# Optimization experiments

Hardware: AMD Instinct MI355X
Metric: run time of the kernel (lower is better)

## Reference

```python
import jax, jax.numpy as jnp
import numpy as np

N, D, V = 2048, 128, 131072
B, T = 8, 256
U_DECAY, X_DECAY, THR = 0.97, 0.97, 0.02


def _ln(z, eps=1e-6):
    # row-wise layernorm matching torch: std with ddof=1 (unbiased)
    m = z.mean(-1, keepdims=True)
    s = jnp.sqrt(((z - m) ** 2).sum(-1, keepdims=True) / (z.shape[-1] - 1))
    return (z - m) / (s + eps)


def setup_inputs() -> dict:
    key = jax.random.key(0)
    k = jax.random.split(key, 5)
    E = jax.random.normal(k[0], (D, N), dtype=jnp.float32) / N ** 0.5
    Dx = jax.random.normal(k[1], (N, D), dtype=jnp.float32) / D ** 0.5
    Dy = jax.random.normal(k[2], (N, D), dtype=jnp.float32) / D ** 0.5
    token_emb = jax.random.normal(k[3], (V, D), dtype=jnp.float32) / D ** 0.5
    tokens = jax.random.randint(k[4], (B, T), 0, V)
    return {"E": E, "Dx": Dx, "Dy": Dy, "token_emb": token_emb, "tokens": tokens}


def reference(E, Dx, Dy, token_emb, tokens):
    Bc, Tc = tokens.shape
    n, d = Dx.shape[0], Dx.shape[1]
    x0 = jnp.zeros((Bc, n), dtype=E.dtype)
    rho0 = jnp.zeros((Bc, d, n), dtype=E.dtype)

    def cell(carry, tok):
        x, rho = carry
        v_prev = token_emb[tok]                             # [B,d]
        xt = X_DECAY * x + v_prev @ Dx.T                    # [B,n]
        xt = xt / (jnp.abs(xt).sum(-1, keepdims=True) + 1e-6)
        thr = THR * xt.max(-1, keepdims=True)
        xt = jnp.where(xt > thr, xt, 0.0)                   # sparsifying threshold
        a_star = jnp.einsum('bdn,bn->bd', rho, xt)          # fast-weight read
        y_core = _ln(a_star) @ Dy.T                         # ln_before_Dy=True -> [B,n]
        yt = jnp.maximum(y_core, 0.0) * jnp.maximum(xt, 0.0)
        v_star = _ln(yt @ E.T)                              # [B,d]
        rho = U_DECAY * (rho + v_prev[:, :, None] * xt[:, None, :])  # rank-1 update + decay
        return (xt, rho), v_star

    (_, _), v_seq = jax.lax.scan(cell, (x0, rho0), tokens.T)  # v_seq: [T,B,d]
    return jnp.transpose(v_seq, (1, 0, 2))                    # [B,T,d]
```

## Files before the change

kernel.cpp:

```cpp
#include <hip/hip_runtime.h>

typedef unsigned int u32;
typedef unsigned short u16;

#define T_SEQ 256
#define N_DIM 2048
#define D_DIM 128
#define B_BATCH 8

typedef __attribute__((ext_vector_type(8))) short bfrag;
typedef __attribute__((ext_vector_type(4))) float f4acc;

__device__ __forceinline__ u16 f2bf(float f) {
  u32 u = __float_as_uint(f);
  return (u16)((u + 0x7FFFu + ((u >> 16) & 1u)) >> 16);
}
__device__ __forceinline__ float bf2f(u16 h) { return __uint_as_float(((u32)h) << 16); }

__global__ __launch_bounds__(128) void k_gather(const float* __restrict__ emb,
                                                const int* __restrict__ toks,
                                                float* __restrict__ Vp) {
  int r = blockIdx.x;
  int d = threadIdx.x;
  int tok = toks[r];
  Vp[(long)r * D_DIM + d] = emb[(long)tok * D_DIM + d];
}

__global__ __launch_bounds__(256) void k_cast(const float* __restrict__ src,
                                              u16* __restrict__ dst, int n) {
  for (int i = blockIdx.x * 256 + threadIdx.x; i < n; i += gridDim.x * 256)
    dst[i] = f2bf(src[i]);
}

__global__ __launch_bounds__(256) void k_zero(float* __restrict__ p, long n4) {
  long i = (long)blockIdx.x * blockDim.x + threadIdx.x;
  if (i < n4) ((float4*)p)[i] = make_float4(0.f, 0.f, 0.f, 0.f);
}

__global__ __launch_bounds__(256) void k_gemm_abT(
    const float* __restrict__ A, const float* __restrict__ Bm, float* __restrict__ C,
    int M, int N, int K) {
  constexpr int BM = 64, BN = 64, BK = 16;
  __shared__ float As[BK][BM + 4];
  __shared__ float Bs[BK][BN + 4];
  int tid = threadIdx.x;
  int tx = tid & 15, ty = tid >> 4;
  int row0 = blockIdx.y * BM, col0 = blockIdx.x * BN;
  float acc[4][4] = {};

  for (int k0 = 0; k0 < K; k0 += BK) {
#pragma unroll
    for (int i = 0; i < 4; i++) {
      int idx = tid + i * 256;
      int m = idx >> 4;
      int k = idx & 15;
      As[k][m] = A[(long)(row0 + m) * K + k0 + k];
      Bs[k][m] = Bm[(long)(col0 + m) * K + k0 + k];
    }
    __syncthreads();
#pragma unroll
    for (int k = 0; k < BK; k++) {
      float a[4], b[4];
#pragma unroll
      for (int i = 0; i < 4; i++) a[i] = As[k][ty * 4 + i];
#pragma unroll
      for (int j = 0; j < 4; j++) b[j] = Bs[k][tx * 4 + j];
#pragma unroll
      for (int i = 0; i < 4; i++)
#pragma unroll
        for (int j = 0; j < 4; j++) acc[i][j] += a[i] * b[j];
    }
    __syncthreads();
  }
#pragma unroll
  for (int i = 0; i < 4; i++) {
    long off = (long)(row0 + ty * 4 + i) * N + col0 + tx * 4;
    *(float4*)(C + off) = make_float4(acc[i][0], acc[i][1], acc[i][2], acc[i][3]);
  }
}

template <int EPI, int TRI>
__global__ __launch_bounds__(256) void k_mfma_abT(
    const u16* __restrict__ A, const u16* __restrict__ Bm, void* __restrict__ Cv,
    const u16* __restrict__ Xr, int M, int N, int K, int KS,
    long sA, long sB, long sC) {
  int bz = blockIdx.z;
  int batch = bz / KS, ks = bz - batch * KS;
  int row0 = blockIdx.y * 64, col0 = blockIdx.x * 64;
  if (TRI && col0 > row0) return;
  A += (long)batch * sA;
  Bm += (long)batch * sB;
  int kLen = K / KS, k0beg = ks * kLen;

  __shared__ __align__(16) u16 As[64 * 64];
  __shared__ __align__(16) u16 Bs[64 * 64];
  int tid = threadIdx.x;
  int w = tid >> 6, lane = tid & 63;
  int qr = (w >> 1) * 32, qc = (w & 1) * 32;
  int l15 = lane & 15, lhi = lane >> 4;

  f4acc acc[2][2];
#pragma unroll
  for (int i = 0; i < 2; i++)
#pragma unroll
    for (int j = 0; j < 2; j++)
#pragma unroll
      for (int e = 0; e < 4; e++) acc[i][j][e] = 0.f;

  for (int k0 = k0beg; k0 < k0beg + kLen; k0 += 64) {
    __syncthreads();
#pragma unroll
    for (int p = 0; p < 2; p++) {
      int idx = tid + p * 256;
      int r = idx >> 3, c8 = (idx & 7) * 8;
      uint4 av = *(const uint4*)(A + (long)(row0 + r) * K + k0 + c8);
      uint4 bv = *(const uint4*)(Bm + (long)(col0 + r) * K + k0 + c8);
      int sw = (c8 * 2) ^ ((r & 7) << 4);
      *(uint4*)((char*)As + r * 128 + sw) = av;
      *(uint4*)((char*)Bs + r * 128 + sw) = bv;
    }
    __syncthreads();
#pragma unroll
    for (int kk = 0; kk < 2; kk++) {
      bfrag af[2], bf[2];
      int cb = kk * 64 + lhi * 16;
#pragma unroll
      for (int f = 0; f < 2; f++) {
        int ra = qr + f * 16 + l15;
        af[f] = *(const bfrag*)((const char*)As + ra * 128 + (cb ^ ((ra & 7) << 4)));
        int rb = qc + f * 16 + l15;
        bf[f] = *(const bfrag*)((const char*)Bs + rb * 128 + (cb ^ ((rb & 7) << 4)));
      }
#pragma unroll
      for (int i = 0; i < 2; i++)
#pragma unroll
        for (int j = 0; j < 2; j++)
          acc[i][j] = __builtin_amdgcn_mfma_f32_16x16x32_bf16(af[i], bf[j], acc[i][j], 0, 0, 0);
    }
  }

#pragma unroll
  for (int i = 0; i < 2; i++)
#pragma unroll
    for (int j = 0; j < 2; j++) {
      int rbase = row0 + qr + i * 16 + lhi * 4;
      int c = col0 + qc + j * 16 + l15;
#pragma unroll
      for (int e = 0; e < 4; e++) {
        long r = rbase + e;
        float v = acc[i][j][e];
        if (EPI == 0) {
          unsafeAtomicAdd((float*)Cv + (long)batch * sC + r * N + c, v);
        } else {
          float xv = bf2f(Xr[r * (long)N + c]);
          ((u16*)Cv)[r * (long)N + c] = f2bf(fmaxf(v, 0.f) * fmaxf(xv, 0.f));
        }
      }
    }
}

template <int CTRL>
__device__ __forceinline__ float dpp_mov(float v) {
  return __int_as_float(
      __builtin_amdgcn_update_dpp(0, __float_as_int(v), CTRL, 0xF, 0xF, true));
}

__device__ __forceinline__ void wave_reduce_sum_max63(float& s, float& m) {
  s += dpp_mov<0x111>(s);  m = fmaxf(m, dpp_mov<0x111>(m));
  s += dpp_mov<0x112>(s);  m = fmaxf(m, dpp_mov<0x112>(m));
  s += dpp_mov<0x114>(s);  m = fmaxf(m, dpp_mov<0x114>(m));
  s += dpp_mov<0x118>(s);  m = fmaxf(m, dpp_mov<0x118>(m));
  s += dpp_mov<0x142>(s);  m = fmaxf(m, dpp_mov<0x142>(m));
  s += dpp_mov<0x143>(s);  m = fmaxf(m, dpp_mov<0x143>(m));
}

__device__ __forceinline__ float wave_sum63(float s) {
  s += dpp_mov<0x111>(s);
  s += dpp_mov<0x112>(s);
  s += dpp_mov<0x114>(s);
  s += dpp_mov<0x118>(s);
  s += dpp_mov<0x142>(s);
  s += dpp_mov<0x143>(s);
  return s;
}

__global__ __launch_bounds__(256) void k_scan(const float* __restrict__ P,
                                              u16* __restrict__ Xb) {
  int b = blockIdx.x;
  int tid = threadIdx.x;
  int wave = tid >> 6;
  int lane = tid & 63;
  __shared__ float red[2][4][2];

  const float4* Pv = (const float4*)(P + (long)b * T_SEQ * N_DIM);
  u16* Xrow = Xb + (long)b * T_SEQ * N_DIM;
  const int ROWQ = N_DIM / 4;
  const long o0 = (long)tid * 2, o1 = o0 + 1;

  float x[8];
#pragma unroll
  for (int j = 0; j < 8; j++) x[j] = 0.f;

  auto rowOff = [&](int t) { return (long)(t < T_SEQ ? t : T_SEQ - 1) * ROWQ; };

  auto step = [&](const float4& v0, const float4& v1, int t) {
    float z[8];
    z[0] = 0.97f * x[0] + v0.x;
    z[1] = 0.97f * x[1] + v0.y;
    z[2] = 0.97f * x[2] + v0.z;
    z[3] = 0.97f * x[3] + v0.w;
    z[4] = 0.97f * x[4] + v1.x;
    z[5] = 0.97f * x[5] + v1.y;
    z[6] = 0.97f * x[6] + v1.z;
    z[7] = 0.97f * x[7] + v1.w;
    float s0 = fabsf(z[0]) + fabsf(z[4]);
    float s1 = fabsf(z[1]) + fabsf(z[5]);
    float s2 = fabsf(z[2]) + fabsf(z[6]);
    float s3 = fabsf(z[3]) + fabsf(z[7]);
    float m0 = fmaxf(z[0], z[4]);
    float m1 = fmaxf(z[1], z[5]);
    float m2 = fmaxf(z[2], z[6]);
    float m3 = fmaxf(z[3], z[7]);
    float s = (s0 + s1) + (s2 + s3);
    float m = fmaxf(fmaxf(m0, m1), fmaxf(m2, m3));
    wave_reduce_sum_max63(s, m);
    int par = t & 1;
    if (lane == 63) {
      red[par][wave][0] = s;
      red[par][wave][1] = m;
    }
    __syncthreads();
    float S = (red[par][0][0] + red[par][1][0]) + (red[par][2][0] + red[par][3][0]);
    float M = fmaxf(fmaxf(red[par][0][1], red[par][1][1]),
                    fmaxf(red[par][2][1], red[par][3][1]));
    float inv = 1.f / (S + 1e-6f);
    float thr = 0.02f * M;
#pragma unroll
    for (int j = 0; j < 8; j++) x[j] = (z[j] > thr) ? z[j] * inv : 0.f;
    uint4 pk;
    pk.x = (u32)f2bf(x[0]) | ((u32)f2bf(x[1]) << 16);
    pk.y = (u32)f2bf(x[2]) | ((u32)f2bf(x[3]) << 16);
    pk.z = (u32)f2bf(x[4]) | ((u32)f2bf(x[5]) << 16);
    pk.w = (u32)f2bf(x[6]) | ((u32)f2bf(x[7]) << 16);
    *(uint4*)(Xrow + (long)t * N_DIM + tid * 8) = pk;
  };

  float4 A0 = Pv[rowOff(0) + o0], A1 = Pv[rowOff(0) + o1];
  float4 B0 = Pv[rowOff(1) + o0], B1 = Pv[rowOff(1) + o1];
  float4 C0 = Pv[rowOff(2) + o0], C1 = Pv[rowOff(2) + o1];
  float4 D0, D1;

  for (int t = 0; t < T_SEQ; t += 4) {
    D0 = Pv[rowOff(t + 3) + o0];
    D1 = Pv[rowOff(t + 3) + o1];
    step(A0, A1, t);
    A0 = Pv[rowOff(t + 4) + o0];
    A1 = Pv[rowOff(t + 4) + o1];
    step(B0, B1, t + 1);
    B0 = Pv[rowOff(t + 5) + o0];
    B1 = Pv[rowOff(t + 5) + o1];
    step(C0, C1, t + 2);
    C0 = Pv[rowOff(t + 6) + o0];
    C1 = Pv[rowOff(t + 6) + o1];
    step(D0, D1, t + 3);
  }
}

__global__ __launch_bounds__(128) void k_astar_ln(const float* __restrict__ S,
                                                  const float* __restrict__ Vp,
                                                  u16* __restrict__ LnAb) {
  int bx = blockIdx.x;
  int b = bx >> 8, t = bx & 255;
  int d = threadIdx.x;
  int wave = d >> 6, lane = d & 63;
  __shared__ float redS[2], redV[2];
  const float* Sb = S + ((long)b * T_SEQ + t) * T_SEQ;
  const float* Vb = Vp + (long)b * T_SEQ * D_DIM;
  float acc = 0.f;
  float w = 1.f;
  for (int s = t - 1; s >= 0; s--) {
    w *= 0.97f;
    acc += w * Sb[s] * Vb[(long)s * D_DIM + d];
  }
  float s1 = wave_sum63(acc);
  if (lane == 63) redS[wave] = s1;
  __syncthreads();
  float mean = (redS[0] + redS[1]) * (1.f / 128.f);
  float dv = acc - mean;
  float v = wave_sum63(dv * dv);
  if (lane == 63) redV[wave] = v;
  __syncthreads();
  float sd = sqrtf((redV[0] + redV[1]) * (1.f / 127.f));
  LnAb[((long)b * T_SEQ + t) * D_DIM + d] = f2bf(dv / (sd + 1e-6f));
}

__global__ __launch_bounds__(64) void k_ln(const float* __restrict__ In,
                                           float* __restrict__ Out) {
  long base = (long)blockIdx.x * D_DIM;
  int lane = threadIdx.x;
  float a = In[base + lane];
  float b = In[base + lane + 64];
  float s = a + b;
#pragma unroll
  for (int off = 32; off >= 1; off >>= 1) s += __shfl_xor(s, off);
  float m = s * (1.f / 128.f);
  float da = a - m, db = b - m;
  float v = da * da + db * db;
#pragma unroll
  for (int off = 32; off >= 1; off >>= 1) v += __shfl_xor(v, off);
  float sd = sqrtf(v * (1.f / 127.f));
  float invs = 1.f / (sd + 1e-6f);
  Out[base + lane] = da * invs;
  Out[base + lane + 64] = db * invs;
}

extern "C" void kernel_launch(void* const* d_in, const int* in_sizes, int n_in,
                              void* d_out, int out_size, void* d_ws, size_t ws_size,
                              hipStream_t stream) {
  const float* E = (const float*)d_in[0];
  const float* Dx = (const float*)d_in[1];
  const float* Dy = (const float*)d_in[2];
  const float* emb = (const float*)d_in[3];
  const int* toks = (const int*)d_in[4];
  float* out = (float*)d_out;

  char* ws = (char*)d_ws;
  const size_t MB = 1u << 20;
  float* Vp = (float*)(ws + 0 * MB);
  float* P = (float*)(ws + 1 * MB);
  u16* Ytb = (u16*)(ws + 1 * MB);
  u16* Xb = (u16*)(ws + 17 * MB);
  float* S = (float*)(ws + 25 * MB);
  float* U = (float*)(ws + 27 * MB);
  u16* LnAb = (u16*)(ws + 28 * MB);
  u16* Dyb = (u16*)(ws + 29 * MB);
  u16* Eb = (u16*)(ws + 30 * MB);

  const int R = B_BATCH * T_SEQ;

  k_gather<<<R, D_DIM, 0, stream>>>(emb, toks, Vp);
  k_cast<<<256, 256, 0, stream>>>(Dy, Dyb, N_DIM * D_DIM);
  k_cast<<<256, 256, 0, stream>>>(E, Eb, N_DIM * D_DIM);
  k_gemm_abT<<<dim3(N_DIM / 64, R / 64, 1), 256, 0, stream>>>(
      Vp, Dx, P, R, N_DIM, D_DIM);
  k_scan<<<B_BATCH, 256, 0, stream>>>(P, Xb);
  k_zero<<<768, 256, 0, stream>>>(S, 3L * MB / 16);
  k_mfma_abT<0, 1><<<dim3(4, 4, B_BATCH * 4), 256, 0, stream>>>(
      Xb, Xb, S, nullptr, T_SEQ, T_SEQ, N_DIM, 4,
      (long)T_SEQ * N_DIM, (long)T_SEQ * N_DIM, (long)T_SEQ * T_SEQ);
  k_astar_ln<<<R, D_DIM, 0, stream>>>(S, Vp, LnAb);
  k_mfma_abT<1, 0><<<dim3(N_DIM / 64, R / 64, 1), 256, 0, stream>>>(
      LnAb, Dyb, Ytb, Xb, R, N_DIM, D_DIM, 1, 0, 0, 0);
  k_mfma_abT<0, 0><<<dim3(D_DIM / 64, R / 64, 8), 256, 0, stream>>>(
      Ytb, Eb, U, nullptr, R, D_DIM, N_DIM, 8, 0, 0, 0);
  k_ln<<<R, 64, 0, stream>>>(U, out);
}
```

Baseline: 297.9 us.

## Use split-bf16 MFMA for P projection and LDS-staged async loads in scan

Replaces the fp32 SIMT GEMM computing V·Dx^T with a bf16 MFMA kernel that splits each operand into high and low bf16 parts and sums three products, keeping accuracy close to fp32. This adds a cast kernel for Dx and writes hi/lo copies in the gather kernel. The serial scan kernel now prefetches rows of P into a triple-buffered LDS ring via global_load_lds, with explicit waitcnt and barriers replacing the register prefetch. The goal is to cut GEMM compute time and hide load latency in the latency-bound scan, at the cost of extra casting passes and hand-managed synchronization.

```diff
diff --git a/kernel.cpp b/kernel.cpp
--- a/kernel.cpp
+++ b/kernel.cpp
@@ -17,13 +17,25 @@
 }
 __device__ __forceinline__ float bf2f(u16 h) { return __uint_as_float(((u32)h) << 16); }
 
+__device__ __forceinline__ void stage16(const void* g, void* l) {
+  __builtin_amdgcn_global_load_lds(
+      (const __attribute__((address_space(1))) void*)g,
+      (__attribute__((address_space(3))) void*)l, 16, 0, 0);
+}
+
 __global__ __launch_bounds__(128) void k_gather(const float* __restrict__ emb,
                                                 const int* __restrict__ toks,
-                                                float* __restrict__ Vp) {
+                                                float* __restrict__ Vp,
+                                                u16* __restrict__ Vph,
+                                                u16* __restrict__ Vpl) {
   int r = blockIdx.x;
   int d = threadIdx.x;
-  int tok = toks[r];
-  Vp[(long)r * D_DIM + d] = emb[(long)tok * D_DIM + d];
+  float v = emb[(long)toks[r] * D_DIM + d];
+  long o = (long)r * D_DIM + d;
+  Vp[o] = v;
+  u16 h = f2bf(v);
+  Vph[o] = h;
+  Vpl[o] = f2bf(v - bf2f(h));
 }
 
 __global__ __launch_bounds__(256) void k_cast(const float* __restrict__ src,
@@ -32,51 +44,91 @@
     dst[i] = f2bf(src[i]);
 }
 
+__global__ __launch_bounds__(256) void k_cast2(const float* __restrict__ src,
+                                               u16* __restrict__ h,
+                                               u16* __restrict__ l, int n) {
+  for (int i = blockIdx.x * 256 + threadIdx.x; i < n; i += gridDim.x * 256) {
+    float v = src[i];
+    u16 hh = f2bf(v);
+    h[i] = hh;
+    l[i] = f2bf(v - bf2f(hh));
+  }
+}
+
 __global__ __launch_bounds__(256) void k_zero(float* __restrict__ p, long n4) {
   long i = (long)blockIdx.x * blockDim.x + threadIdx.x;
   if (i < n4) ((float4*)p)[i] = make_float4(0.f, 0.f, 0.f, 0.f);
 }
 
-__global__ __launch_bounds__(256) void k_gemm_abT(
-    const float* __restrict__ A, const float* __restrict__ Bm, float* __restrict__ C,
-    int M, int N, int K) {
-  constexpr int BM = 64, BN = 64, BK = 16;
-  __shared__ float As[BK][BM + 4];
-  __shared__ float Bs[BK][BN + 4];
+__global__ __launch_bounds__(256) void k_mfma_p(
+    const u16* __restrict__ Ah, const u16* __restrict__ Al,
+    const u16* __restrict__ Bh, const u16* __restrict__ Bl,
+    float* __restrict__ C) {
+  __shared__ __align__(16) u16 sA[2][64 * 128];
+  __shared__ __align__(16) u16 sB[2][64 * 128];
   int tid = threadIdx.x;
-  int tx = tid & 15, ty = tid >> 4;
-  int row0 = blockIdx.y * BM, col0 = blockIdx.x * BN;
-  float acc[4][4] = {};
-
-  for (int k0 = 0; k0 < K; k0 += BK) {
-#pragma unroll
-    for (int i = 0; i < 4; i++) {
-      int idx = tid + i * 256;
-      int m = idx >> 4;
-      int k = idx & 15;
-      As[k][m] = A[(long)(row0 + m) * K + k0 + k];
-      Bs[k][m] = Bm[(long)(col0 + m) * K + k0 + k];
-    }
-    __syncthreads();
-#pragma unroll
-    for (int k = 0; k < BK; k++) {
-      float a[4], b[4];
-#pragma unroll
-      for (int i = 0; i < 4; i++) a[i] = As[k][ty * 4 + i];
-#pragma unroll
-      for (int j = 0; j < 4; j++) b[j] = Bs[k][tx * 4 + j];
-#pragma unroll
-      for (int i = 0; i < 4; i++)
-#pragma unroll
-        for (int j = 0; j < 4; j++) acc[i][j] += a[i] * b[j];
-    }
-    __syncthreads();
-  }
-#pragma unroll
-  for (int i = 0; i < 4; i++) {
-    long off = (long)(row0 + ty * 4 + i) * N + col0 + tx * 4;
-    *(float4*)(C + off) = make_float4(acc[i][0], acc[i][1], acc[i][2], acc[i][3]);
-  }
+  int w = tid >> 6, lane = tid & 63;
+  int qr = (w >> 1) * 32, qc = (w & 1) * 32;
+  int l15 = lane & 15, lhi = lane >> 4;
+  int row0 = blockIdx.y * 64, col0 = blockIdx.x * 64;
+
+  f4acc acc[2][2];
+#pragma unroll
+  for (int i = 0; i < 2; i++)
+#pragma unroll
+    for (int j = 0; j < 2; j++)
+#pragma unroll
+      for (int e = 0; e < 4; e++) acc[i][j][e] = 0.f;
+
+#pragma unroll
+  for (int hl = 0; hl < 2; hl++) {
+    const u16* A = hl ? Al : Ah;
+    const u16* B = hl ? Bl : Bh;
+#pragma unroll
+    for (int p = 0; p < 4; p++) {
+      int idx = tid + p * 256;
+      int r = idx >> 4, ch = idx & 15;
+      int off = r * 256 + ((ch * 16) ^ ((r & 7) << 4));
+      *(uint4*)((char*)sA[hl] + off) = *(const uint4*)(A + (long)(row0 + r) * D_DIM + ch * 8);
+      *(uint4*)((char*)sB[hl] + off) = *(const uint4*)(B + (long)(col0 + r) * D_DIM + ch * 8);
+    }
+  }
+  __syncthreads();
+
+#pragma unroll
+  for (int kk = 0; kk < 4; kk++) {
+    bfrag ah[2], al[2], bh[2], bl[2];
+    int cb = kk * 64 + lhi * 16;
+#pragma unroll
+    for (int f = 0; f < 2; f++) {
+      int ra = qr + f * 16 + l15, rb = qc + f * 16 + l15;
+      int oa = ra * 256 + (cb ^ ((ra & 7) << 4));
+      int ob = rb * 256 + (cb ^ ((rb & 7) << 4));
+      ah[f] = *(const bfrag*)((const char*)sA[0] + oa);
+      al[f] = *(const bfrag*)((const char*)sA[1] + oa);
+      bh[f] = *(const bfrag*)((const char*)sB[0] + ob);
+      bl[f] = *(const bfrag*)((const char*)sB[1] + ob);
+    }
+#pragma unroll
+    for (int i = 0; i < 2; i++)
+#pragma unroll
+      for (int j = 0; j < 2; j++) {
+        acc[i][j] = __builtin_amdgcn_mfma_f32_16x16x32_bf16(ah[i], bh[j], acc[i][j], 0, 0, 0);
+        acc[i][j] = __builtin_amdgcn_mfma_f32_16x16x32_bf16(ah[i], bl[j], acc[i][j], 0, 0, 0);
+        acc[i][j] = __builtin_amdgcn_mfma_f32_16x16x32_bf16(al[i], bh[j], acc[i][j], 0, 0, 0);
+      }
+  }
+
+#pragma unroll
+  for (int i = 0; i < 2; i++)
+#pragma unroll
+    for (int j = 0; j < 2; j++) {
+      int rbase = row0 + qr + i * 16 + lhi * 4;
+      int c = col0 + qc + j * 16 + l15;
+#pragma unroll
+      for (int e = 0; e < 4; e++)
+        C[(long)(rbase + e) * N_DIM + c] = acc[i][j][e];
+    }
 }
 
 template <int EPI, int TRI>
@@ -190,20 +242,37 @@
   int tid = threadIdx.x;
   int wave = tid >> 6;
   int lane = tid & 63;
-  __shared__ float red[2][4][2];
-
-  const float4* Pv = (const float4*)(P + (long)b * T_SEQ * N_DIM);
+  __shared__ __align__(16) float buf[3][N_DIM];
+  __shared__ __align__(16) float red[2][4][2];
+
+  const float* Prow = P + (long)b * T_SEQ * N_DIM;
   u16* Xrow = Xb + (long)b * T_SEQ * N_DIM;
-  const int ROWQ = N_DIM / 4;
-  const long o0 = (long)tid * 2, o1 = o0 + 1;
+  const int wq = wave * 512;
+  const float* gsrc0 = Prow + wq + lane * 4;
 
   float x[8];
 #pragma unroll
   for (int j = 0; j < 8; j++) x[j] = 0.f;
 
-  auto rowOff = [&](int t) { return (long)(t < T_SEQ ? t : T_SEQ - 1) * ROWQ; };
-
-  auto step = [&](const float4& v0, const float4& v1, int t) {
+  stage16(gsrc0, &buf[0][wq]);
+  stage16(gsrc0 + 256, &buf[0][wq + 256]);
+  stage16(gsrc0 + N_DIM, &buf[1][wq]);
+  stage16(gsrc0 + N_DIM + 256, &buf[1][wq + 256]);
+  asm volatile("s_waitcnt vmcnt(2)" ::: "memory");
+  __builtin_amdgcn_sched_barrier(0);
+
+  int cur = 0;
+  for (int t = 0; t < T_SEQ; ++t) {
+    int nsl = cur + 2; if (nsl >= 3) nsl -= 3;
+    int tp = (t + 2 < T_SEQ) ? t + 2 : T_SEQ - 1;
+    const float* src = gsrc0 + (long)tp * N_DIM;
+    stage16(src, &buf[nsl][wq]);
+    stage16(src + 256, &buf[nsl][wq + 256]);
+    asm volatile("s_waitcnt vmcnt(5)" ::: "memory");
+    __builtin_amdgcn_sched_barrier(0);
+
+    float4 v0 = *(const float4*)&buf[cur][tid * 8];
+    float4 v1 = *(const float4*)&buf[cur][tid * 8 + 4];
     float z[8];
     z[0] = 0.97f * x[0] + v0.x;
     z[1] = 0.97f * x[1] + v0.y;
@@ -229,7 +298,7 @@
       red[par][wave][0] = s;
       red[par][wave][1] = m;
     }
-    __syncthreads();
+    asm volatile("s_waitcnt lgkmcnt(0)\n\ts_barrier" ::: "memory");
     float S = (red[par][0][0] + red[par][1][0]) + (red[par][2][0] + red[par][3][0]);
     float M = fmaxf(fmaxf(red[par][0][1], red[par][1][1]),
                     fmaxf(red[par][2][1], red[par][3][1]));
@@ -243,26 +312,7 @@
     pk.z = (u32)f2bf(x[4]) | ((u32)f2bf(x[5]) << 16);
     pk.w = (u32)f2bf(x[6]) | ((u32)f2bf(x[7]) << 16);
     *(uint4*)(Xrow + (long)t * N_DIM + tid * 8) = pk;
-  };
-
-  float4 A0 = Pv[rowOff(0) + o0], A1 = Pv[rowOff(0) + o1];
-  float4 B0 = Pv[rowOff(1) + o0], B1 = Pv[rowOff(1) + o1];
-  float4 C0 = Pv[rowOff(2) + o0], C1 = Pv[rowOff(2) + o1];
-  float4 D0, D1;
-
-  for (int t = 0; t < T_SEQ; t += 4) {
-    D0 = Pv[rowOff(t + 3) + o0];
-    D1 = Pv[rowOff(t + 3) + o1];
-    step(A0, A1, t);
-    A0 = Pv[rowOff(t + 4) + o0];
-    A1 = Pv[rowOff(t + 4) + o1];
-    step(B0, B1, t + 1);
-    B0 = Pv[rowOff(t + 5) + o0];
-    B1 = Pv[rowOff(t + 5) + o1];
-    step(C0, C1, t + 2);
-    C0 = Pv[rowOff(t + 6) + o0];
-    C1 = Pv[rowOff(t + 6) + o1];
-    step(D0, D1, t + 3);
+    cur = cur + 1; if (cur == 3) cur = 0;
   }
 }
 
@@ -335,14 +385,18 @@
   u16* LnAb = (u16*)(ws + 28 * MB);
   u16* Dyb = (u16*)(ws + 29 * MB);
   u16* Eb = (u16*)(ws + 30 * MB);
+  u16* Vph = (u16*)(ws + 31 * MB);
+  u16* Vpl = (u16*)(ws + 31 * MB + 512 * 1024);
+  u16* Dxh = (u16*)(ws + 32 * MB);
+  u16* Dxl = (u16*)(ws + 32 * MB + 512 * 1024);
 
   const int R = B_BATCH * T_SEQ;
 
-  k_gather<<<R, D_DIM, 0, stream>>>(emb, toks, Vp);
+  k_gather<<<R, D_DIM, 0, stream>>>(emb, toks, Vp, Vph, Vpl);
   k_cast<<<256, 256, 0, stream>>>(Dy, Dyb, N_DIM * D_DIM);
   k_cast<<<256, 256, 0, stream>>>(E, Eb, N_DIM * D_DIM);
-  k_gemm_abT<<<dim3(N_DIM / 64, R / 64, 1), 256, 0, stream>>>(
-      Vp, Dx, P, R, N_DIM, D_DIM);
+  k_cast2<<<256, 256, 0, stream>>>(Dx, Dxh, Dxl, N_DIM * D_DIM);
+  k_mfma_p<<<dim3(N_DIM / 64, R / 64), 256, 0, stream>>>(Vph, Vpl, Dxh, Dxl, P);
   k_scan<<<B_BATCH, 256, 0, stream>>>(P, Xb);
   k_zero<<<768, 256, 0, stream>>>(S, 3L * MB / 16);
   k_mfma_abT<0, 1><<<dim3(4, 4, B_BATCH * 4), 256, 0, stream>>>(
```

Result: slower. 383.4 us (+28.7%).
